# Kernel tuning notes

Hardware: AMD Instinct MI355X
Metric: run time of the kernel (lower is better)

## Reference

```python
import jax, jax.numpy as jnp
import numpy as np

# model hyperparameters (from init_kwargs 'model' mapping)
SIG = 10.0       # kernel length scale
C = 0.0          # energy integration constant
STD = 1.0        # normalization std
M, N_ATOMS = 64, 24
T_ROWS, DESC = 6000, N_ATOMS * (N_ATOMS - 1) // 2  # 276


def setup_inputs() -> dict:
    key = jax.random.key(0)
    k1, k2, k3 = jax.random.split(key, 3)
    # spread atoms out so pairwise distances are O(1..10) Angstrom-like
    Rs = jax.random.normal(k1, (M, N_ATOMS, 3), jnp.float32) * 3.0
    # training descriptors are inverse distances -> positive values in (0,1)
    xs_train = jax.random.uniform(k2, (T_ROWS, DESC), jnp.float32)
    Jx_alphas = jax.random.normal(k3, (T_ROWS, DESC), jnp.float32) * 0.1
    return {"Rs": Rs, "xs_train": xs_train, "Jx_alphas": Jx_alphas}


def reference(Rs, xs_train, Jx_alphas):
    sig = SIG
    q = np.sqrt(5.0) / sig
    m, n = Rs.shape[0], Rs.shape[1]
    i, j = np.tril_indices(n, k=-1)  # lower-triangular atom pairs, P entries

    # pairwise coordinate differences [M, N, N, 3]
    diffs = Rs[:, :, None, :] - Rs[:, None, :, :]
    # inverse pairwise distances over tril pairs -> descriptor xs [M, P]
    d_ij = jnp.linalg.norm(diffs[:, i, j, :], axis=-1)
    xs = 1.0 / d_ij

    # descriptor differences to all (permuted) training points [M, T, P]
    x_diffs = q * xs[:, None, :] - q * xs_train[None, :, :]
    x_dists = jnp.linalg.norm(x_diffs, axis=-1)            # [M, T]
    exp_xs = (5.0 / (3.0 * sig ** 2)) * jnp.exp(-x_dists)  # [M, T]
    dot = jnp.einsum('mtp,tp->mt', x_diffs, Jx_alphas)     # [M, T]
    exp1 = exp_xs * (1.0 + x_dists)                        # [M, T]

    F1 = jnp.einsum('mt,mtp->mp', exp_xs * dot, x_diffs)   # [M, P]
    F2 = exp1 @ Jx_alphas                                  # [M, P]
    Fs_x = (F1 - F2) * xs ** 3                             # [M, P]

    # scatter pair forces back onto the symmetric [N, N] pair grid;
    # diagonal diffs are zero so leaving mult=0 there matches the original
    mult = jnp.zeros((m, n, n), Rs.dtype)
    mult = mult.at[:, i, j].set(Fs_x).at[:, j, i].set(Fs_x)
    Fs = (diffs * mult[..., None]).sum(axis=1) * STD       # [M, N, 3]

    Es = (exp1 * dot).sum(axis=-1) / q * STD + C           # [M]
    return Es, Fs
```

## Files before the change

### kernel.cpp

```cpp
#include <hip/hip_runtime.h>
#include <math.h>

#define MM 64
#define NA 24
#define NP 276
#define NT 6000
#define NTP 6048
#define QC 0.22360679774997896f
#define EXPC 0.01666666666666667f

#define OFF_XST  0
#define OFF_UU   17664
#define OFF_ES   17728
#define OFF_SW   17792
#define OFF_SH   17856
#define OFF_WT   300480
#define OFF_ET   687552
#define ZTOT     282752

__device__ __forceinline__ float f4c(const float4& v, int i) {
  return i == 0 ? v.x : i == 1 ? v.y : i == 2 ? v.z : v.w;
}

__global__ __launch_bounds__(256) void k_pre(const float* __restrict__ Rs,
                                             float* __restrict__ ws) {
  const int tid = threadIdx.x;
  for (int z = blockIdx.x * 256 + tid; z < ZTOT; z += gridDim.x * 256)
    ws[OFF_ES + z] = 0.f;
  for (int z = blockIdx.x * 256 + tid; z < 6144; z += gridDim.x * 256) {
    if (z < 3072) ws[OFF_WT + 384000 + z] = 0.f;
    else          ws[OFF_ET + 384000 + (z - 3072)] = 0.f;
  }
  if (blockIdx.x < MM) {
    const int m = blockIdx.x;
    __shared__ float sR[NA * 3];
    __shared__ float sAcc[4];
    if (tid < NA * 3) sR[tid] = Rs[m * NA * 3 + tid];
    __syncthreads();
    float acc = 0.f;
    for (int p = tid; p < NP; p += 256) {
      int i = (int)((1.0f + sqrtf(1.0f + 8.0f * (float)p)) * 0.5f);
      while (i * (i - 1) / 2 > p) i--;
      while ((i + 1) * i / 2 <= p) i++;
      int j = p - i * (i - 1) / 2;
      float dx = sR[i * 3 + 0] - sR[j * 3 + 0];
      float dy = sR[i * 3 + 1] - sR[j * 3 + 1];
      float dz = sR[i * 3 + 2] - sR[j * 3 + 2];
      float u = 1.0f / sqrtf(dx * dx + dy * dy + dz * dz);
      ws[OFF_XST + p * 64 + m] = u;
      acc += u * u;
    }
    for (int off = 32; off; off >>= 1) acc += __shfl_down(acc, off);
    if ((tid & 63) == 0) sAcc[tid >> 6] = acc;
    __syncthreads();
    if (tid == 0) ws[OFF_UU + m] = sAcc[0] + sAcc[1] + sAcc[2] + sAcc[3];
  }
}

#define G1_BS 280
#define G1_AS 36
__global__ __launch_bounds__(256, 2) void k_g1(const float* __restrict__ xt,
                                               const float* __restrict__ Ja,
                                               float* __restrict__ ws) {
  __shared__ __align__(16) float2 Bs[16][G1_BS];
  __shared__ __align__(16) float As[NP][G1_AS];
  __shared__ float sVV[16], sC1[16];
  __shared__ float sEsW[4][32], sSwW[4][32];
  const int tid = threadIdx.x;
  const int t0 = blockIdx.x * 16;
  const int m0 = blockIdx.y * 32;

  for (int idx = tid; idx < 16 * 69; idx += 256) {
    const int row = idx / 69;
    const int kq = (idx - row * 69) * 4;
    const float4 v = *(const float4*)(xt + (size_t)(t0 + row) * NP + kq);
    const float4 j = *(const float4*)(Ja + (size_t)(t0 + row) * NP + kq);
    *(float4*)&Bs[row][kq]     = make_float4(v.x, j.x, v.y, j.y);
    *(float4*)&Bs[row][kq + 2] = make_float4(v.z, j.z, v.w, j.w);
  }
  for (int idx = tid; idx < NP * 8; idx += 256) {
    const int p = idx >> 3;
    const int mq = (idx & 7) * 4;
    *(float4*)&As[p][mq] = *(const float4*)(ws + OFF_XST + p * 64 + m0 + mq);
  }
  const int r = tid & 15;
  const int c = tid >> 4;
  const float2 uu2 = *(const float2*)(ws + OFF_UU + m0 + 2 * r);
  __syncthreads();

  {
    const int tl = tid >> 4;
    const int l16 = tid & 15;
    float a = 0.f, b = 0.f;
    for (int k = l16; k < NP; k += 16) {
      const float2 x = Bs[tl][k];
      a = fmaf(x.x, x.x, a);
      b = fmaf(x.x, x.y, b);
    }
#pragma unroll
    for (int off = 8; off; off >>= 1) {
      a += __shfl_down(a, off, 16);
      b += __shfl_down(b, off, 16);
    }
    if (l16 == 0) { sVV[tl] = a; sC1[tl] = b; }
  }
  __syncthreads();

  float av0 = 0.f, av1 = 0.f, aj0 = 0.f, aj1 = 0.f;
#pragma unroll 4
  for (int kk = 0; kk < NP; kk += 2) {
    const float4 b  = *(const float4*)&Bs[c][kk];
    const float2 a0 = *(const float2*)&As[kk][2 * r];
    const float2 a1 = *(const float2*)&As[kk + 1][2 * r];
    av0 = fmaf(a0.x, b.x, av0); aj0 = fmaf(a0.x, b.y, aj0);
    av1 = fmaf(a0.y, b.x, av1); aj1 = fmaf(a0.y, b.y, aj1);
    av0 = fmaf(a1.x, b.z, av0); aj0 = fmaf(a1.x, b.w, aj0);
    av1 = fmaf(a1.y, b.z, av1); aj1 = fmaf(a1.y, b.w, aj1);
  }

  const float vvt = sVV[c];
  const float c1t = sC1[c];
  float es2[2], sw2[2], wv[2], ev[2];
#pragma unroll
  for (int i = 0; i < 2; i++) {
    const float g1v = i ? av1 : av0;
    const float g2v = i ? aj1 : aj0;
    const float uum = i ? uu2.y : uu2.x;
    float d2 = fmaxf(uum - 2.f * g1v + vvt, 0.f);
    float xd = QC * sqrtf(d2);
    float dv = QC * (g2v - c1t);
    float ex = EXPC * __expf(-xd);
    float e1v = ex * (1.f + xd);
    float w_ = ex * dv;
    wv[i] = w_; ev[i] = e1v;
    es2[i] = e1v * dv;
    sw2[i] = w_;
  }
  const int t = t0 + c;
  *(float2*)(ws + OFF_WT + (size_t)t * 64 + m0 + 2 * r) = make_float2(wv[0], wv[1]);
  *(float2*)(ws + OFF_ET + (size_t)t * 64 + m0 + 2 * r) = make_float2(ev[0], ev[1]);

#pragma unroll
  for (int i = 0; i < 2; i++) {
    es2[i] += __shfl_down(es2[i], 32); es2[i] += __shfl_down(es2[i], 16);
    sw2[i] += __shfl_down(sw2[i], 32); sw2[i] += __shfl_down(sw2[i], 16);
  }
  const int w = tid >> 6;
  if ((tid & 63) < 16) {
    sEsW[w][2 * r + 0] = es2[0]; sEsW[w][2 * r + 1] = es2[1];
    sSwW[w][2 * r + 0] = sw2[0]; sSwW[w][2 * r + 1] = sw2[1];
  }
  __syncthreads();
  if (tid < 32) {
    const float es = sEsW[0][tid] + sEsW[1][tid] + sEsW[2][tid] + sEsW[3][tid];
    const float sw = sSwW[0][tid] + sSwW[1][tid] + sSwW[2][tid] + sSwW[3][tid];
    atomicAdd(ws + OFF_ES + m0 + tid, es);
    atomicAdd(ws + OFF_SW + m0 + tid, sw);
  }
}

#define G2_KC 96
__global__ __launch_bounds__(256, 2) void k_g2(const float* __restrict__ xt,
                                               const float* __restrict__ Ja,
                                               float* __restrict__ ws) {
  __shared__ __align__(16) float Aw[G2_KC][68];
  __shared__ __align__(16) float Ae[G2_KC][68];
  __shared__ __align__(16) float2 Bvj[G2_KC][18];
  const int tid = threadIdx.x;
  const int p0 = blockIdx.x * 16;
  const int k0 = blockIdx.y * G2_KC;
  const int validp = (NP - p0 < 16) ? (NP - p0) : 16;

  for (int idx = tid; idx < G2_KC * 16; idx += 256) {
    const int k = idx >> 4;
    const int mq = (idx & 15) * 4;
    *(float4*)&Aw[k][mq] = *(const float4*)(ws + OFF_WT + (size_t)(k0 + k) * 64 + mq);
    *(float4*)&Ae[k][mq] = *(const float4*)(ws + OFF_ET + (size_t)(k0 + k) * 64 + mq);
  }
  for (int idx = tid; idx < G2_KC * 4; idx += 256) {
    const int k = idx >> 2;
    const int pq = (idx & 3) * 4;
    const int t = k0 + k;
    float4 v = make_float4(0.f, 0.f, 0.f, 0.f), j = v;
    if (pq < validp && t < NT) {
      v = *(const float4*)(xt + (size_t)t * NP + p0 + pq);
      j = *(const float4*)(Ja + (size_t)t * NP + p0 + pq);
    }
    *(float4*)&Bvj[k][pq]     = make_float4(v.x, j.x, v.y, j.y);
    *(float4*)&Bvj[k][pq + 2] = make_float4(v.z, j.z, v.w, j.w);
  }
  __syncthreads();

  const int r = tid & 31;
  const int c = tid >> 5;
  float f1[2][2] = {{0.f, 0.f}, {0.f, 0.f}};
  float f2[2][2] = {{0.f, 0.f}, {0.f, 0.f}};
#pragma unroll 4
  for (int k = 0; k < G2_KC; k++) {
    const float2 aw = *(const float2*)&Aw[k][2 * r];
    const float2 ae = *(const float2*)&Ae[k][2 * r];
    const float4 b  = *(const float4*)&Bvj[k][2 * c];
    f1[0][0] = fmaf(aw.x, b.x, f1[0][0]); f1[0][1] = fmaf(aw.x, b.z, f1[0][1]);
    f1[1][0] = fmaf(aw.y, b.x, f1[1][0]); f1[1][1] = fmaf(aw.y, b.z, f1[1][1]);
    f2[0][0] = fmaf(ae.x, b.y, f2[0][0]); f2[0][1] = fmaf(ae.x, b.w, f2[0][1]);
    f2[1][0] = fmaf(ae.y, b.y, f2[1][0]); f2[1][1] = fmaf(ae.y, b.w, f2[1][1]);
  }

  const int sh = blockIdx.y & 7;
  float* b1 = ws + OFF_SH + (size_t)(sh * 2 + 0) * NP * 64;
  float* b2 = ws + OFF_SH + (size_t)(sh * 2 + 1) * NP * 64;
#pragma unroll
  for (int j = 0; j < 2; j++) {
    const int pl = 2 * c + j;
    if (pl < validp) {
      const int p = p0 + pl;
#pragma unroll
      for (int i = 0; i < 2; i++) {
        atomicAdd(b1 + (size_t)p * 64 + 2 * r + i, f1[i][j]);
        atomicAdd(b2 + (size_t)p * 64 + 2 * r + i, f2[i][j]);
      }
    }
  }
}

__global__ __launch_bounds__(320) void k_final(const float* __restrict__ Rs,
                                               const float* __restrict__ ws,
                                               float* __restrict__ out) {
  const int m = blockIdx.x;
  const int tid = threadIdx.x;
  __shared__ float fx[NP];
  __shared__ float sR[NA * 3];
  if (tid < NA * 3) sR[tid] = Rs[m * NA * 3 + tid];
  const float sw = ws[OFF_SW + m];
  for (int p = tid; p < NP; p += 320) {
    float f1p = 0.f, f2 = 0.f;
#pragma unroll
    for (int s = 0; s < 8; s++) {
      f1p += ws[OFF_SH + ((size_t)(s * 2 + 0) * NP + p) * 64 + m];
      f2  += ws[OFF_SH + ((size_t)(s * 2 + 1) * NP + p) * 64 + m];
    }
    const float u = ws[OFF_XST + p * 64 + m];
    const float F1 = QC * (u * sw - f1p);
    fx[p] = (F1 - f2) * u * u * u;
  }
  __syncthreads();
  if (tid == 0) out[m] = ws[OFF_ES + m] / QC;
  if (tid < NA * 3) {
    const int a = tid / 3, cc = tid % 3;
    const float ra = sR[a * 3 + cc];
    float acc = 0.f;
    for (int b = 0; b < NA; b++) {
      if (b == a) continue;
      const int i = a > b ? a : b, j = a > b ? b : a;
      const int p = i * (i - 1) / 2 + j;
      acc += (sR[b * 3 + cc] - ra) * fx[p];
    }
    out[MM + m * NA * 3 + tid] = acc;
  }
}

extern "C" void kernel_launch(void* const* d_in, const int* in_sizes, int n_in,
                              void* d_out, int out_size, void* d_ws, size_t ws_size,
                              hipStream_t stream) {
  const float* Rs = (const float*)d_in[0];
  const float* xt = (const float*)d_in[1];
  const float* Ja = (const float*)d_in[2];
  float* out = (float*)d_out;
  float* ws = (float*)d_ws;

  k_pre<<<128, 256, 0, stream>>>(Rs, ws);
  k_g1<<<dim3(375, 2), 256, 0, stream>>>(xt, Ja, ws);
  k_g2<<<dim3(18, 63), 256, 0, stream>>>(xt, Ja, ws);
  k_final<<<MM, 320, 0, stream>>>(Rs, ws, out);
}
```

Measured before the change: 137.1 us.

## Use split-bf16 MFMA for descriptor Gram products in k_g1

Moves the per-(m,t) dot products in k_g1 from scalar FP32 FMAs onto bf16 MFMA instructions. Precision is recovered with a hi/lo split that keeps three cross terms. k_pre now also converts xs, xs_train and Jx_alphas into padded hi/lo bf16 arrays and computes the per-row norms and Ja dot products. This adds an extra global pass writing about 4x bf16 copies of the training data and slightly lower accuracy, in exchange for matrix-core throughput in the first GEMM stage.

```diff
diff --git a/kernel.cpp b/kernel.cpp
--- a/kernel.cpp
+++ b/kernel.cpp
@@ -6,31 +6,56 @@
 #define NP 276
 #define NT 6000
 #define NTP 6048
+#define NKP 288
 #define QC 0.22360679774997896f
 #define EXPC 0.01666666666666667f
 
 #define OFF_XST  0
 #define OFF_UU   17664
-#define OFF_ES   17728
-#define OFF_SW   17792
-#define OFF_SH   17856
-#define OFF_WT   300480
-#define OFF_ET   687552
+#define OFF_VV   17728
+#define OFF_C1   23728
+#define OFF_ES   29728
+#define OFF_SW   29792
+#define OFF_SH   29856
+#define OFF_WT   312480
+#define OFF_ET   699552
+#define OFF_XHL  1086624
 #define ZTOT     282752
-
+#define U_XSH 0
+#define U_XSL 18432
+#define U_XTH 36864
+#define U_XTL 1764864
+#define U_JAH 3492864
+#define U_JAL 5220864
+
+typedef __attribute__((ext_vector_type(8))) short bf16x8;
+typedef __attribute__((ext_vector_type(4))) float f32x4;
+
+__device__ __forceinline__ unsigned short f2bf(float x) {
+  unsigned int u = __float_as_uint(x);
+  unsigned int r = (u + 0x7FFFu + ((u >> 16) & 1u)) >> 16;
+  return (unsigned short)r;
+}
+__device__ __forceinline__ float bf2f(unsigned short h) {
+  return __uint_as_float(((unsigned int)h) << 16);
+}
 __device__ __forceinline__ float f4c(const float4& v, int i) {
   return i == 0 ? v.x : i == 1 ? v.y : i == 2 ? v.z : v.w;
 }
 
 __global__ __launch_bounds__(256) void k_pre(const float* __restrict__ Rs,
+                                             const float* __restrict__ xt,
+                                             const float* __restrict__ Ja,
                                              float* __restrict__ ws) {
   const int tid = threadIdx.x;
+  unsigned short* bfw = (unsigned short*)(ws + OFF_XHL);
   for (int z = blockIdx.x * 256 + tid; z < ZTOT; z += gridDim.x * 256)
     ws[OFF_ES + z] = 0.f;
   for (int z = blockIdx.x * 256 + tid; z < 6144; z += gridDim.x * 256) {
     if (z < 3072) ws[OFF_WT + 384000 + z] = 0.f;
     else          ws[OFF_ET + 384000 + (z - 3072)] = 0.f;
   }
+
   if (blockIdx.x < MM) {
     const int m = blockIdx.x;
     __shared__ float sR[NA * 3];
@@ -38,124 +63,155 @@
     if (tid < NA * 3) sR[tid] = Rs[m * NA * 3 + tid];
     __syncthreads();
     float acc = 0.f;
-    for (int p = tid; p < NP; p += 256) {
-      int i = (int)((1.0f + sqrtf(1.0f + 8.0f * (float)p)) * 0.5f);
-      while (i * (i - 1) / 2 > p) i--;
-      while ((i + 1) * i / 2 <= p) i++;
-      int j = p - i * (i - 1) / 2;
-      float dx = sR[i * 3 + 0] - sR[j * 3 + 0];
-      float dy = sR[i * 3 + 1] - sR[j * 3 + 1];
-      float dz = sR[i * 3 + 2] - sR[j * 3 + 2];
-      float u = 1.0f / sqrtf(dx * dx + dy * dy + dz * dz);
-      ws[OFF_XST + p * 64 + m] = u;
-      acc += u * u;
+    for (int p = tid; p < NKP; p += 256) {
+      float u = 0.f;
+      if (p < NP) {
+        int i = (int)((1.0f + sqrtf(1.0f + 8.0f * (float)p)) * 0.5f);
+        while (i * (i - 1) / 2 > p) i--;
+        while ((i + 1) * i / 2 <= p) i++;
+        int j = p - i * (i - 1) / 2;
+        float dx = sR[i * 3 + 0] - sR[j * 3 + 0];
+        float dy = sR[i * 3 + 1] - sR[j * 3 + 1];
+        float dz = sR[i * 3 + 2] - sR[j * 3 + 2];
+        u = 1.0f / sqrtf(dx * dx + dy * dy + dz * dz);
+        ws[OFF_XST + p * 64 + m] = u;
+        acc += u * u;
+      }
+      const unsigned short hi = f2bf(u);
+      const unsigned short lo = f2bf(u - bf2f(hi));
+      bfw[U_XSH + m * NKP + p] = hi;
+      bfw[U_XSL + m * NKP + p] = lo;
     }
     for (int off = 32; off; off >>= 1) acc += __shfl_down(acc, off);
     if ((tid & 63) == 0) sAcc[tid >> 6] = acc;
     __syncthreads();
     if (tid == 0) ws[OFF_UU + m] = sAcc[0] + sAcc[1] + sAcc[2] + sAcc[3];
-  }
-}
-
-#define G1_BS 280
-#define G1_AS 36
-__global__ __launch_bounds__(256, 2) void k_g1(const float* __restrict__ xt,
-                                               const float* __restrict__ Ja,
-                                               float* __restrict__ ws) {
-  __shared__ __align__(16) float2 Bs[16][G1_BS];
-  __shared__ __align__(16) float As[NP][G1_AS];
-  __shared__ float sVV[16], sC1[16];
-  __shared__ float sEsW[4][32], sSwW[4][32];
+  } else {
+    const int t = (blockIdx.x - MM) * 4 + (tid >> 6);
+    const int lane = tid & 63;
+    float a = 0.f, b = 0.f;
+#pragma unroll
+    for (int it = 0; it < 3; it++) {
+      const int k = lane * 2 + it * 128;
+      if (k < NKP) {
+        float2 v = make_float2(0.f, 0.f), j = v;
+        if (k < NP) {
+          v = *(const float2*)(xt + (size_t)t * NP + k);
+          j = *(const float2*)(Ja + (size_t)t * NP + k);
+          a += v.x * v.x + v.y * v.y;
+          b += v.x * j.x + v.y * j.y;
+        }
+        unsigned short vh0 = f2bf(v.x), vh1 = f2bf(v.y);
+        unsigned short jh0 = f2bf(j.x), jh1 = f2bf(j.y);
+        *(ushort2*)(bfw + U_XTH + (size_t)t * NKP + k) = make_ushort2(vh0, vh1);
+        *(ushort2*)(bfw + U_XTL + (size_t)t * NKP + k) =
+            make_ushort2(f2bf(v.x - bf2f(vh0)), f2bf(v.y - bf2f(vh1)));
+        *(ushort2*)(bfw + U_JAH + (size_t)t * NKP + k) = make_ushort2(jh0, jh1);
+        *(ushort2*)(bfw + U_JAL + (size_t)t * NKP + k) =
+            make_ushort2(f2bf(j.x - bf2f(jh0)), f2bf(j.y - bf2f(jh1)));
+      }
+    }
+    for (int off = 32; off; off >>= 1) {
+      a += __shfl_down(a, off);
+      b += __shfl_down(b, off);
+    }
+    if (lane == 0) { ws[OFF_VV + t] = a; ws[OFF_C1 + t] = b; }
+  }
+}
+
+#define SA_HI 0
+#define SA_LO 9472
+#define SB_XH 18944
+#define SB_XL 23680
+#define SB_JH 28416
+#define SB_JL 33152
+#define S_US  37888
+__global__ __launch_bounds__(128, 2) void k_g1(float* __restrict__ ws) {
+  __shared__ __align__(16) unsigned short smem[S_US];
   const int tid = threadIdx.x;
   const int t0 = blockIdx.x * 16;
   const int m0 = blockIdx.y * 32;
-
-  for (int idx = tid; idx < 16 * 69; idx += 256) {
-    const int row = idx / 69;
-    const int kq = (idx - row * 69) * 4;
-    const float4 v = *(const float4*)(xt + (size_t)(t0 + row) * NP + kq);
-    const float4 j = *(const float4*)(Ja + (size_t)(t0 + row) * NP + kq);
-    *(float4*)&Bs[row][kq]     = make_float4(v.x, j.x, v.y, j.y);
-    *(float4*)&Bs[row][kq + 2] = make_float4(v.z, j.z, v.w, j.w);
-  }
-  for (int idx = tid; idx < NP * 8; idx += 256) {
-    const int p = idx >> 3;
-    const int mq = (idx & 7) * 4;
-    *(float4*)&As[p][mq] = *(const float4*)(ws + OFF_XST + p * 64 + m0 + mq);
-  }
-  const int r = tid & 15;
-  const int c = tid >> 4;
-  const float2 uu2 = *(const float2*)(ws + OFF_UU + m0 + 2 * r);
+  const unsigned short* bfw = (const unsigned short*)(ws + OFF_XHL);
+
+  for (int idx = tid; idx < 2304; idx += 128) {
+    const int arr = idx / 1152;
+    const int rem = idx - arr * 1152;
+    const int row = rem / 36, c = rem - row * 36;
+    const unsigned short* src = bfw + (arr ? U_XSL : U_XSH) + (size_t)(m0 + row) * NKP + c * 8;
+    *(uint4*)&smem[(arr ? SA_LO : SA_HI) + row * 296 + c * 8] = *(const uint4*)src;
+  }
+  for (int idx = tid; idx < 2304; idx += 128) {
+    const int arr = idx / 576;
+    const int rem = idx - arr * 576;
+    const int row = rem / 36, c = rem - row * 36;
+    const int ubase = (arr == 0) ? U_XTH : (arr == 1) ? U_XTL : (arr == 2) ? U_JAH : U_JAL;
+    const int sbase = SB_XH + arr * 4736;
+    const unsigned short* src = bfw + ubase + (size_t)(t0 + row) * NKP + c * 8;
+    *(uint4*)&smem[sbase + row * 296 + c * 8] = *(const uint4*)src;
+  }
   __syncthreads();
 
-  {
-    const int tl = tid >> 4;
-    const int l16 = tid & 15;
-    float a = 0.f, b = 0.f;
-    for (int k = l16; k < NP; k += 16) {
-      const float2 x = Bs[tl][k];
-      a = fmaf(x.x, x.x, a);
-      b = fmaf(x.x, x.y, b);
-    }
-#pragma unroll
-    for (int off = 8; off; off >>= 1) {
-      a += __shfl_down(a, off, 16);
-      b += __shfl_down(b, off, 16);
-    }
-    if (l16 == 0) { sVV[tl] = a; sC1[tl] = b; }
-  }
-  __syncthreads();
-
-  float av0 = 0.f, av1 = 0.f, aj0 = 0.f, aj1 = 0.f;
-#pragma unroll 4
-  for (int kk = 0; kk < NP; kk += 2) {
-    const float4 b  = *(const float4*)&Bs[c][kk];
-    const float2 a0 = *(const float2*)&As[kk][2 * r];
-    const float2 a1 = *(const float2*)&As[kk + 1][2 * r];
-    av0 = fmaf(a0.x, b.x, av0); aj0 = fmaf(a0.x, b.y, aj0);
-    av1 = fmaf(a0.y, b.x, av1); aj1 = fmaf(a0.y, b.y, aj1);
-    av0 = fmaf(a1.x, b.z, av0); aj0 = fmaf(a1.x, b.w, aj0);
-    av1 = fmaf(a1.y, b.z, av1); aj1 = fmaf(a1.y, b.w, aj1);
-  }
-
-  const float vvt = sVV[c];
-  const float c1t = sC1[c];
-  float es2[2], sw2[2], wv[2], ev[2];
-#pragma unroll
-  for (int i = 0; i < 2; i++) {
-    const float g1v = i ? av1 : av0;
-    const float g2v = i ? aj1 : aj0;
-    const float uum = i ? uu2.y : uu2.x;
-    float d2 = fmaxf(uum - 2.f * g1v + vvt, 0.f);
+  const int ln = tid & 63, w = tid >> 6;
+  const int tcol = ln & 15;
+  const int qr = ln >> 4;
+  const int aoff = (w * 16 + tcol) * 296 + qr * 8;
+  const int boff = tcol * 296 + qr * 8;
+
+  f32x4 accv = {0.f, 0.f, 0.f, 0.f};
+  f32x4 accj = {0.f, 0.f, 0.f, 0.f};
+#pragma unroll
+  for (int ks = 0; ks < 9; ks++) {
+    const int k0 = ks * 32;
+    const bf16x8 ah  = *(const bf16x8*)&smem[SA_HI + aoff + k0];
+    const bf16x8 al  = *(const bf16x8*)&smem[SA_LO + aoff + k0];
+    const bf16x8 bxh = *(const bf16x8*)&smem[SB_XH + boff + k0];
+    const bf16x8 bxl = *(const bf16x8*)&smem[SB_XL + boff + k0];
+    const bf16x8 bjh = *(const bf16x8*)&smem[SB_JH + boff + k0];
+    const bf16x8 bjl = *(const bf16x8*)&smem[SB_JL + boff + k0];
+    accv = __builtin_amdgcn_mfma_f32_16x16x32_bf16(ah, bxh, accv, 0, 0, 0);
+    accv = __builtin_amdgcn_mfma_f32_16x16x32_bf16(ah, bxl, accv, 0, 0, 0);
+    accv = __builtin_amdgcn_mfma_f32_16x16x32_bf16(al, bxh, accv, 0, 0, 0);
+    accj = __builtin_amdgcn_mfma_f32_16x16x32_bf16(ah, bjh, accj, 0, 0, 0);
+    accj = __builtin_amdgcn_mfma_f32_16x16x32_bf16(ah, bjl, accj, 0, 0, 0);
+    accj = __builtin_amdgcn_mfma_f32_16x16x32_bf16(al, bjh, accj, 0, 0, 0);
+  }
+
+  const int m = m0 + w * 16 + qr * 4;
+  const int t = t0 + tcol;
+  const float4 uu4 = *(const float4*)(ws + OFF_UU + m);
+  const float vvt = ws[OFF_VV + t];
+  const float c1t = ws[OFF_C1 + t];
+  float wq[4], eq[4], es4[4], sw4[4];
+#pragma unroll
+  for (int i = 0; i < 4; i++) {
+    const float g1v = accv[i];
+    const float g2v = accj[i];
+    float d2 = fmaxf(f4c(uu4, i) - 2.f * g1v + vvt, 0.f);
     float xd = QC * sqrtf(d2);
     float dv = QC * (g2v - c1t);
     float ex = EXPC * __expf(-xd);
     float e1v = ex * (1.f + xd);
     float w_ = ex * dv;
-    wv[i] = w_; ev[i] = e1v;
-    es2[i] = e1v * dv;
-    sw2[i] = w_;
-  }
-  const int t = t0 + c;
-  *(float2*)(ws + OFF_WT + (size_t)t * 64 + m0 + 2 * r) = make_float2(wv[0], wv[1]);
-  *(float2*)(ws + OFF_ET + (size_t)t * 64 + m0 + 2 * r) = make_float2(ev[0], ev[1]);
-
-#pragma unroll
-  for (int i = 0; i < 2; i++) {
-    es2[i] += __shfl_down(es2[i], 32); es2[i] += __shfl_down(es2[i], 16);
-    sw2[i] += __shfl_down(sw2[i], 32); sw2[i] += __shfl_down(sw2[i], 16);
-  }
-  const int w = tid >> 6;
-  if ((tid & 63) < 16) {
-    sEsW[w][2 * r + 0] = es2[0]; sEsW[w][2 * r + 1] = es2[1];
-    sSwW[w][2 * r + 0] = sw2[0]; sSwW[w][2 * r + 1] = sw2[1];
-  }
-  __syncthreads();
-  if (tid < 32) {
-    const float es = sEsW[0][tid] + sEsW[1][tid] + sEsW[2][tid] + sEsW[3][tid];
-    const float sw = sSwW[0][tid] + sSwW[1][tid] + sSwW[2][tid] + sSwW[3][tid];
-    atomicAdd(ws + OFF_ES + m0 + tid, es);
-    atomicAdd(ws + OFF_SW + m0 + tid, sw);
+    wq[i] = w_; eq[i] = e1v;
+    es4[i] = e1v * dv;
+    sw4[i] = w_;
+  }
+  *(float4*)(ws + OFF_WT + (size_t)t * 64 + m) = make_float4(wq[0], wq[1], wq[2], wq[3]);
+  *(float4*)(ws + OFF_ET + (size_t)t * 64 + m) = make_float4(eq[0], eq[1], eq[2], eq[3]);
+#pragma unroll
+  for (int off = 8; off; off >>= 1) {
+#pragma unroll
+    for (int i = 0; i < 4; i++) {
+      es4[i] += __shfl_down(es4[i], off, 16);
+      sw4[i] += __shfl_down(sw4[i], off, 16);
+    }
+  }
+  if (tcol == 0) {
+#pragma unroll
+    for (int i = 0; i < 4; i++) {
+      atomicAdd(ws + OFF_ES + m + i, es4[i]);
+      atomicAdd(ws + OFF_SW + m + i, sw4[i]);
+    }
   }
 }
 
@@ -268,8 +324,8 @@
   float* out = (float*)d_out;
   float* ws = (float*)d_ws;
 
-  k_pre<<<128, 256, 0, stream>>>(Rs, ws);
-  k_g1<<<dim3(375, 2), 256, 0, stream>>>(xt, Ja, ws);
+  k_pre<<<MM + NT / 4, 256, 0, stream>>>(Rs, xt, Ja, ws);
+  k_g1<<<dim3(375, 2), 128, 0, stream>>>(ws);
   k_g2<<<dim3(18, 63), 256, 0, stream>>>(xt, Ja, ws);
   k_final<<<MM, 320, 0, stream>>>(Rs, ws, out);
 }
```

New measurement: 166.7 us. 1.22x slower.
